# Kernel optimization log

Measured on AMD Instinct MI355X. Metric: run time of the kernel, lower is better.

Reference implementation:

```python
import jax, jax.numpy as jnp
import numpy as np

ALPHA = 0.0257
DELTA_T = 3.0
SOURCE_INTENSITY = 100000.0
MASK_THRESHOLD = 1000.0


def _laplace_kernel():
    # 7-point 3D Laplacian stencil, shape [O=1, I=1, 3, 3, 3]
    k = np.zeros((1, 1, 3, 3, 3), dtype=np.float32)
    k[0, 0, 1, 1, 1] = -6.0
    k[0, 0, 0, 1, 1] = 1.0
    k[0, 0, 2, 1, 1] = 1.0
    k[0, 0, 1, 0, 1] = 1.0
    k[0, 0, 1, 2, 1] = 1.0
    k[0, 0, 1, 1, 0] = 1.0
    k[0, 0, 1, 1, 2] = 1.0
    return jnp.asarray(k)


def setup_inputs() -> dict:
    key = jax.random.key(0)
    k1, k2 = jax.random.split(key)
    shape = (8, 1, 128, 128, 128)  # [B, C=1, D, H, W]
    model_output = jax.random.normal(k1, shape, dtype=jnp.float32)
    current_input = jax.random.normal(k2, shape, dtype=jnp.float32)
    return {"model_output": model_output, "current_input": current_input}


def reference(model_output, current_input):
    kernel = _laplace_kernel().astype(current_input.dtype)
    # zero-padded 3x3x3 depthwise (C=1) Laplacian stencil
    laplacian = jax.lax.conv_general_dilated(
        current_input, kernel,
        window_strides=(1, 1, 1),
        padding=[(1, 1), (1, 1), (1, 1)],
        dimension_numbers=("NCDHW", "OIDHW", "NCDHW"),
    )
    temporal_derivative = (model_output - current_input) / DELTA_T
    source_term = jnp.where(current_input > MASK_THRESHOLD,
                            jnp.asarray(SOURCE_INTENSITY, current_input.dtype),
                            jnp.asarray(0.0, current_input.dtype))
    residual = temporal_derivative - ALPHA * laplacian - source_term
    return jnp.mean(residual * residual)
```

## Files before the change

### kernel.cpp

```cpp
#include <hip/hip_runtime.h>


constexpr int WW = 128;
constexpr int HH = 128;
constexpr int DD = 128;
constexpr int PLANE = HH * WW;
constexpr long long N_ELEM = 8LL * DD * HH * WW;
constexpr int ZCHUNK = 16;
constexpr int NBLOCKS = 8 * 16 * (DD / ZCHUNK);

constexpr float ALPHA  = 0.0257f;
constexpr float INV_DT = 1.0f / 3.0f;
constexpr float SRC_I  = 100000.0f;
constexpr float THRESH = 1000.0f;

typedef float f32x4 __attribute__((ext_vector_type(4)));

struct L4 { float4 zp, m, ym, yp; };

__device__ __forceinline__ float4 ldg4(const float* p) {
    return *reinterpret_cast<const float4*>(p);
}
__device__ __forceinline__ float4 ldnt4(const float* p) {
    f32x4 v = __builtin_nontemporal_load(reinterpret_cast<const f32x4*>(p));
    return make_float4(v.x, v.y, v.z, v.w);
}

__device__ __forceinline__ L4 load_step(const float* __restrict__ cur,
                                        const float* __restrict__ model,
                                        int i, int ozp, int oym, int oyp) {
    L4 t;
    t.zp = ldg4(cur + i + ozp);
    t.m  = ldnt4(model + i);
    t.ym = ldg4(cur + i + oym);
    t.yp = ldg4(cur + i + oyp);
    return t;
}

__device__ __forceinline__ float sq_residual4(
        const float4 c, const float4 m,
        const float4 ym, const float4 yp,
        const float4 zm, const float4 zp,
        const float fym, const float fyp, const float fzm, const float fzp,
        const bool x_lo, const bool x_hi, float acc) {
    float left  = __shfl_up(c.w, 1, 64);
    float right = __shfl_down(c.x, 1, 64);
    if (x_lo) left = 0.0f;
    if (x_hi) right = 0.0f;

    const float cc[4]  = {c.x, c.y, c.z, c.w};
    const float mm[4]  = {m.x, m.y, m.z, m.w};
    const float xs[6]  = {left, c.x, c.y, c.z, c.w, right};
    const float yms[4] = {ym.x, ym.y, ym.z, ym.w};
    const float yps[4] = {yp.x, yp.y, yp.z, yp.w};
    const float zms[4] = {zm.x, zm.y, zm.z, zm.w};
    const float zps[4] = {zp.x, zp.y, zp.z, zp.w};

    #pragma unroll
    for (int j = 0; j < 4; ++j) {
        float lap = xs[j] + xs[j + 2] - 6.0f * cc[j];
        lap = fmaf(fym, yms[j], lap);
        lap = fmaf(fyp, yps[j], lap);
        lap = fmaf(fzm, zms[j], lap);
        lap = fmaf(fzp, zps[j], lap);
        const float td  = (mm[j] - cc[j]) * INV_DT;
        const float src = (cc[j] > THRESH) ? SRC_I : 0.0f;
        const float r   = td - ALPHA * lap - src;
        acc = fmaf(r, r, acc);
    }
    return acc;
}

__global__ __launch_bounds__(256) void heat_loss_kernel(
        const float* __restrict__ model,
        const float* __restrict__ cur,
        float* __restrict__ block_sums) {
    const int bx = blockIdx.x;
    const int zc = bx & 7;
    const int ys = (bx >> 3) & 15;
    const int b  = bx >> 7;
    const int z0 = zc * ZCHUNK;

    const int x4 = threadIdx.x & 31;
    const int yr = threadIdx.x >> 5;
    const int y  = ys * 8 + yr;

    const bool x_lo = (x4 == 0);
    const bool x_hi = (x4 == 31);
    const float fym = (y == 0)   ? 0.0f : 1.0f;
    const float fyp = (y == 127) ? 0.0f : 1.0f;
    const int oym = (y == 0)   ? 0 : -WW;
    const int oyp = (y == 127) ? 0 :  WW;

    int i = ((b * DD + z0) * HH + y) * WW + x4 * 4;

    const int ozm0 = (z0 == 0) ? 0 : -PLANE;
    float fzm = (z0 == 0) ? 0.0f : 1.0f;
    float4 zm = ldg4(cur + i + ozm0);
    float4 c  = ldg4(cur + i);

    L4 t0 = load_step(cur, model, i, PLANE, oym, oyp);

    float acc = 0.0f;

    #pragma unroll 1
    for (int s = 0; s < ZCHUNK - 1; ++s) {
        const int zz1 = z0 + s + 1;
        const int ozp1 = (zz1 == 127) ? 0 : PLANE;
        L4 t1 = load_step(cur, model, i + PLANE, ozp1, oym, oyp);

        __builtin_amdgcn_sched_barrier(0);

        acc = sq_residual4(c, t0.m, t0.ym, t0.yp, zm, t0.zp,
                           fym, fyp, fzm, 1.0f, x_lo, x_hi, acc);
        zm = c;
        c  = t0.zp;
        fzm = 1.0f;
        t0 = t1;
        i += PLANE;
    }

    const float fzp_last = (z0 + ZCHUNK - 1 == 127) ? 0.0f : 1.0f;
    acc = sq_residual4(c, t0.m, t0.ym, t0.yp, zm, t0.zp,
                       fym, fyp, fzm, fzp_last, x_lo, x_hi, acc);

    #pragma unroll
    for (int off = 32; off > 0; off >>= 1)
        acc += __shfl_down(acc, off, 64);

    __shared__ float wsum[4];
    const int lane = threadIdx.x & 63;
    const int wave = threadIdx.x >> 6;
    if (lane == 0) wsum[wave] = acc;
    __syncthreads();

    if (threadIdx.x == 0)
        block_sums[blockIdx.x] = wsum[0] + wsum[1] + wsum[2] + wsum[3];
}

__global__ __launch_bounds__(256) void finalize_kernel(
        const float* __restrict__ block_sums, float* __restrict__ out) {
    double a = 0.0;
    for (int j = threadIdx.x; j < NBLOCKS; j += 256)
        a += (double)block_sums[j];

    #pragma unroll
    for (int off = 32; off > 0; off >>= 1)
        a += __shfl_down(a, off, 64);

    __shared__ double wsum[4];
    const int lane = threadIdx.x & 63;
    const int wave = threadIdx.x >> 6;
    if (lane == 0) wsum[wave] = a;
    __syncthreads();

    if (threadIdx.x == 0)
        out[0] = (float)((wsum[0] + wsum[1] + wsum[2] + wsum[3]) / (double)N_ELEM);
}

extern "C" void kernel_launch(void* const* d_in, const int* in_sizes, int n_in,
                              void* d_out, int out_size, void* d_ws, size_t ws_size,
                              hipStream_t stream) {
    const float* model = (const float*)d_in[0];
    const float* cur   = (const float*)d_in[1];
    float* block_sums = (float*)d_ws;
    float* out = (float*)d_out;

    heat_loss_kernel<<<NBLOCKS, 256, 0, stream>>>(model, cur, block_sums);
    finalize_kernel<<<1, 256, 0, stream>>>(block_sums, out);
}
```

Baseline: 134.6 us.

## Share y-neighbor rows through double-buffered LDS instead of redundant global loads

Each block now stages its 8 current-plane rows plus two halo rows in a double-buffered shared-memory tile and reads the y-1 and y+1 neighbors from LDS. Before, every thread issued two extra global float4 loads per z step for those neighbors. This reduces global/L2 load instructions per z step from four to about two per thread. In exchange it adds a block-wide barrier every z step, LDS write/read traffic, and a per-wave branch for the halo loads.

```diff
diff --git a/kernel.cpp b/kernel.cpp
--- a/kernel.cpp
+++ b/kernel.cpp
@@ -16,25 +16,12 @@
 
 typedef float f32x4 __attribute__((ext_vector_type(4)));
 
-struct L4 { float4 zp, m, ym, yp; };
-
 __device__ __forceinline__ float4 ldg4(const float* p) {
     return *reinterpret_cast<const float4*>(p);
 }
 __device__ __forceinline__ float4 ldnt4(const float* p) {
     f32x4 v = __builtin_nontemporal_load(reinterpret_cast<const f32x4*>(p));
     return make_float4(v.x, v.y, v.z, v.w);
-}
-
-__device__ __forceinline__ L4 load_step(const float* __restrict__ cur,
-                                        const float* __restrict__ model,
-                                        int i, int ozp, int oym, int oyp) {
-    L4 t;
-    t.zp = ldg4(cur + i + ozp);
-    t.m  = ldnt4(model + i);
-    t.ym = ldg4(cur + i + oym);
-    t.yp = ldg4(cur + i + oyp);
-    return t;
 }
 
 __device__ __forceinline__ float sq_residual4(
@@ -81,60 +68,90 @@
     const int b  = bx >> 7;
     const int z0 = zc * ZCHUNK;
 
-    const int x4 = threadIdx.x & 31;
-    const int yr = threadIdx.x >> 5;
+    const int tid = threadIdx.x;
+    const int x4 = tid & 31;
+    const int yr = tid >> 5;
     const int y  = ys * 8 + yr;
 
     const bool x_lo = (x4 == 0);
     const bool x_hi = (x4 == 31);
     const float fym = (y == 0)   ? 0.0f : 1.0f;
     const float fyp = (y == 127) ? 0.0f : 1.0f;
-    const int oym = (y == 0)   ? 0 : -WW;
-    const int oyp = (y == 127) ? 0 :  WW;
+
+    __shared__ __align__(16) float lds[2][10][128];
 
     int i = ((b * DD + z0) * HH + y) * WW + x4 * 4;
 
-    const int ozm0 = (z0 == 0) ? 0 : -PLANE;
+    const bool has_edge = (tid < 64);
+    int ei = 0;
+    int erow_lds = 0;
+    if (has_edge) {
+        int ey = (tid < 32) ? (ys * 8 - 1) : (ys * 8 + 8);
+        ey = min(127, max(0, ey));
+        erow_lds = (tid < 32) ? 0 : 9;
+        ei = ((b * DD + z0) * HH + ey) * WW + (tid & 31) * 4;
+    }
+
     float fzm = (z0 == 0) ? 0.0f : 1.0f;
-    float4 zm = ldg4(cur + i + ozm0);
+    float4 zm = ldg4(cur + i + ((z0 == 0) ? 0 : -PLANE));
     float4 c  = ldg4(cur + i);
+    float4 zp0 = ldg4(cur + i + PLANE);
+    float4 m0  = ldnt4(model + i);
+    float4 e0;
+    if (has_edge) e0 = ldg4(cur + ei);
 
-    L4 t0 = load_step(cur, model, i, PLANE, oym, oyp);
+    *reinterpret_cast<float4*>(&lds[0][yr + 1][x4 * 4]) = c;
+    if (has_edge) *reinterpret_cast<float4*>(&lds[0][erow_lds][(tid & 31) * 4]) = e0;
+    __syncthreads();
 
     float acc = 0.0f;
+    int cb = 0;
 
     #pragma unroll 1
     for (int s = 0; s < ZCHUNK - 1; ++s) {
-        const int zz1 = z0 + s + 1;
-        const int ozp1 = (zz1 == 127) ? 0 : PLANE;
-        L4 t1 = load_step(cur, model, i + PLANE, ozp1, oym, oyp);
+        const int ozp = (z0 + s + 2 > 127) ? 0 : PLANE;
+        float4 zp1 = ldg4(cur + i + PLANE + ozp);
+        float4 m1  = ldnt4(model + i + PLANE);
+        float4 e1;
+        if (has_edge) e1 = ldg4(cur + ei + PLANE);
 
         __builtin_amdgcn_sched_barrier(0);
 
-        acc = sq_residual4(c, t0.m, t0.ym, t0.yp, zm, t0.zp,
+        const float4 ym = *reinterpret_cast<const float4*>(&lds[cb][yr][x4 * 4]);
+        const float4 yp = *reinterpret_cast<const float4*>(&lds[cb][yr + 2][x4 * 4]);
+
+        acc = sq_residual4(c, m0, ym, yp, zm, zp0,
                            fym, fyp, fzm, 1.0f, x_lo, x_hi, acc);
-        zm = c;
-        c  = t0.zp;
-        fzm = 1.0f;
-        t0 = t1;
+
+        zm = c; c = zp0; fzm = 1.0f;
+        zp0 = zp1; m0 = m1;
+        *reinterpret_cast<float4*>(&lds[cb ^ 1][yr + 1][x4 * 4]) = c;
+        if (has_edge) *reinterpret_cast<float4*>(&lds[cb ^ 1][erow_lds][(tid & 31) * 4]) = e1;
+        cb ^= 1;
         i += PLANE;
+        ei += PLANE;
+        __syncthreads();
     }
 
-    const float fzp_last = (z0 + ZCHUNK - 1 == 127) ? 0.0f : 1.0f;
-    acc = sq_residual4(c, t0.m, t0.ym, t0.yp, zm, t0.zp,
-                       fym, fyp, fzm, fzp_last, x_lo, x_hi, acc);
+    {
+        const float4 ym = *reinterpret_cast<const float4*>(&lds[cb][yr][x4 * 4]);
+        const float4 yp = *reinterpret_cast<const float4*>(&lds[cb][yr + 2][x4 * 4]);
+        const float fzp_last = (z0 + ZCHUNK - 1 == 127) ? 0.0f : 1.0f;
+        acc = sq_residual4(c, m0, ym, yp, zm, zp0,
+                           fym, fyp, fzm, fzp_last, x_lo, x_hi, acc);
+    }
 
     #pragma unroll
     for (int off = 32; off > 0; off >>= 1)
         acc += __shfl_down(acc, off, 64);
 
     __shared__ float wsum[4];
-    const int lane = threadIdx.x & 63;
-    const int wave = threadIdx.x >> 6;
+    const int lane = tid & 63;
+    const int wave = tid >> 6;
     if (lane == 0) wsum[wave] = acc;
     __syncthreads();
 
-    if (threadIdx.x == 0)
+    if (tid == 0)
         block_sums[blockIdx.x] = wsum[0] + wsum[1] + wsum[2] + wsum[3];
 }
 
```

After: 131.3 us. 1.03x faster.
